# Optimization experiments

Hardware: AMD Instinct MI355X
Metric: run time of the kernel (lower is better)

The kernel has to match this reference:

```python
import jax, jax.numpy as jnp
import numpy as np

E = 8      # num_experts
D = 512    # input feature dim
H1 = 512   # expert_hidden[0]
H2 = 256   # expert_hidden[1]
Y = 256    # y_dim
B = 8192   # batch
ALPHA = 0.2


def setup_inputs() -> dict:
    key = jax.random.key(0)
    ks = jax.random.split(key, 8)
    h = jax.random.normal(ks[0], (B, D), dtype=jnp.float32)
    gate_id = jax.random.randint(ks[1], (B,), 0, E, dtype=jnp.int64)
    # Per-expert MLP parameters, stacked over expert axis (Glorot-ish scale)
    W1 = jax.random.normal(ks[2], (E, D, H1), dtype=jnp.float32) * (1.0 / np.sqrt(D))
    b1 = jnp.zeros((E, H1), dtype=jnp.float32)
    W2 = jax.random.normal(ks[3], (E, H1, H2), dtype=jnp.float32) * (1.0 / np.sqrt(H1))
    b2 = jnp.zeros((E, H2), dtype=jnp.float32)
    W3 = jax.random.normal(ks[4], (E, H2, Y), dtype=jnp.float32) * (1.0 / np.sqrt(H2))
    b3 = jnp.zeros((E, Y), dtype=jnp.float32)
    return {"h": h, "gate_id": gate_id, "W1": W1, "b1": b1,
            "W2": W2, "b2": b2, "W3": W3, "b3": b3}


def _leaky(x):
    return jnp.where(x > 0, x, ALPHA * x)


def reference(h, gate_id, W1, b1, W2, b2, W3, b3):
    # Hard routing: gate_id = clip(round(gate_id), 0, E-1)
    g = jnp.clip(jnp.round(gate_id.astype(jnp.float32)).astype(jnp.int32), 0, E - 1)
    # Dense all-experts compute (jit-friendly, no dynamic shapes), then select
    # the routed expert's output per row. Same math as dispatch/stitch.
    a1 = _leaky(jnp.einsum('bd,edh->ebh', h, W1) + b1[:, None, :])   # [E,B,H1]
    a2 = _leaky(jnp.einsum('ebh,ehk->ebk', a1, W2) + b2[:, None, :]) # [E,B,H2]
    y = jnp.einsum('ebk,eky->eby', a2, W3) + b3[:, None, :]          # [E,B,Y]
    out = y[g, jnp.arange(h.shape[0])]                                # [B,Y]
    return out
```

## Files before the change

kernel.cpp:

```cpp
#include <hip/hip_runtime.h>
#include <stdint.h>

#define NE 8
#define ND 512
#define NH1 512
#define NH2 256
#define NY 256
#define NB 8192
#define BM3 32
#define MAXT3 (NB/BM3 + NE - 1)
#define W1T (NE * (ND/32) * (NH1/32))
#define W2T (NE * (NH1/32) * (NH2/32))
#define W3T (NE * (NH2/32) * (NY/32))
#define WTT (W1T + W2T + W3T)

typedef float f32x4 __attribute__((ext_vector_type(4)));
typedef __bf16 bf16x8 __attribute__((ext_vector_type(8)));
typedef unsigned short u16x8 __attribute__((ext_vector_type(8)));

__device__ __forceinline__ unsigned short f2bf(float f) {
  unsigned int u = __float_as_uint(f);
  u += 0x7fffu + ((u >> 16) & 1u);
  return (unsigned short)(u >> 16);
}

__device__ __forceinline__ int clampe(int g) {
  return g < 0 ? 0 : (g > NE - 1 ? NE - 1 : g);
}



__global__ __launch_bounds__(1024)
void prep_k(const int* __restrict__ gate,
            const float* __restrict__ W1, const float* __restrict__ W2,
            const float* __restrict__ W3,
            unsigned short* __restrict__ w1f, unsigned short* __restrict__ w2f,
            unsigned short* __restrict__ w3f,
            int* __restrict__ meta, int* __restrict__ perm)
{
  __shared__ char sm[36928] __attribute__((aligned(16)));
  int b = blockIdx.x, t = threadIdx.x;

  if (b < WTT) {
    float* tt = (float*)sm;
    const float* src; unsigned short* dst; int K, N, idx;
    if (b < W1T)            { src = W1; dst = w1f; K = ND;  N = NH1; idx = b; }
    else if (b < W1T + W2T) { src = W2; dst = w2f; K = NH1; N = NH2; idx = b - W1T; }
    else                    { src = W3; dst = w3f; K = NH2; N = NY;  idx = b - W1T - W2T; }
    int ntn = N >> 5, ntk = K >> 5;
    int n0 = (idx % ntn) * 32;
    int k0 = ((idx / ntn) % ntk) * 32;
    int g  = idx / (ntn * ntk);
    int tx = t & 31, ty = t >> 5;
    const float* s = src + (size_t)g * K * N;
    tt[ty * 33 + tx] = s[(size_t)(k0 + ty) * N + n0 + tx];
    __syncthreads();
    unsigned short* d = dst + (size_t)g * K * N;
    int j    = t & 7;
    int lane = (t >> 3) & 63;
    int fi   = t >> 9;
    int c    = ((lane >> 4) << 3) | j;
    int i    = (fi << 4) | (lane & 15);
    int kt   = k0 >> 5;
    int f    = (n0 >> 4) + fi;
    d[(((size_t)kt * (N >> 4) + f) * 64 + lane) * 8 + j] = f2bf(tt[c * 33 + i]);
    return;
  }

  unsigned int* lcnt = (unsigned int*)sm;
  int* pre   = (int*)(sm + 4096);
  int* cnt8  = (int*)(sm + 36864);
  int* offs8 = cnt8 + 8;

  int g8[8];
  unsigned int c = 0;
  #pragma unroll
  for (int i = 0; i < 8; i++) {
    int g = clampe(gate[t * 8 + i]);
    g8[i] = g;
    c += 1u << (4 * g);
  }
  lcnt[t] = c;
  __syncthreads();

  int wave = t >> 6, lane = t & 63;
  if (wave < NE) {
    int e = wave;
    int carry = 0;
    for (int ch = 0; ch < 16; ch++) {
      int idx = ch * 64 + lane;
      int v = (int)((lcnt[idx] >> (4 * e)) & 15u);
      int s = v;
      #pragma unroll
      for (int d = 1; d < 64; d <<= 1) {
        int up = __shfl_up(s, d, 64);
        if (lane >= d) s += up;
      }
      pre[e * 1024 + idx] = carry + s - v;
      carry += __shfl(s, 63, 64);
    }
    if (lane == 0) cnt8[e] = carry;
  }
  __syncthreads();

  if (t == 0) {
    int off = 0, tt2 = 0;
    for (int e = 0; e < NE; e++) {
      int cc = cnt8[e];
      meta[e] = cc;
      meta[8 + e] = off;
      offs8[e] = off;
      int ntl = (cc + BM3 - 1) / BM3;
      for (int i = 0; i < ntl; i++) meta[1024 + tt2++] = (e << 16) | i;
      off += cc;
    }
    meta[24] = tt2;
  }
  __syncthreads();

  unsigned int run = 0;
  #pragma unroll
  for (int i = 0; i < 8; i++) {
    int g = g8[i];
    int r = (int)((run >> (4 * g)) & 15u);
    run += 1u << (4 * g);
    perm[offs8[g] + pre[g * 1024 + t] + r] = t * 8 + i;
  }
}

__global__ __launch_bounds__(512, 4)
void mlp_k(const float* __restrict__ h,
           const float* __restrict__ b1, const float* __restrict__ b2,
           const float* __restrict__ b3,
           float* __restrict__ out,
           const int* __restrict__ meta, const int* __restrict__ perm,
           const unsigned short* __restrict__ w1f,
           const unsigned short* __restrict__ w2f,
           const unsigned short* __restrict__ w3f)
{
  __shared__ unsigned short sA[BM3 * 520];
  __shared__ unsigned short sB[BM3 * 520];
  __shared__ int permc[BM3];

  if ((int)blockIdx.x >= meta[24]) return;

  int tid  = threadIdx.x;
  int ent  = meta[1024 + blockIdx.x];
  int e    = ent >> 16;
  int trow = ent & 0xffff;
  int cnt  = meta[e];
  int off  = meta[8 + e];
  int row0 = trow * BM3;

  if (tid < BM3) {
    int grow = row0 + tid;
    permc[tid] = (grow < cnt) ? perm[off + grow] : 0;
  }
  __syncthreads();

  int wave = tid >> 6, lane = tid & 63;
  int lm = lane & 15, quad = lane >> 4;

  {
    int r  = tid >> 4;
    int cb = (tid & 15) * 8;
    const float* hrow = h + (size_t)permc[r] * ND;
    #pragma unroll
    for (int jj = 0; jj < 4; jj++) {
      int col = cb + jj * 128;
      float4 f0 = *(const float4*)(hrow + col);
      float4 f1 = *(const float4*)(hrow + col + 4);
      union { u16x8 v; unsigned short u[8]; } pk;
      pk.u[0] = f2bf(f0.x); pk.u[1] = f2bf(f0.y); pk.u[2] = f2bf(f0.z); pk.u[3] = f2bf(f0.w);
      pk.u[4] = f2bf(f1.x); pk.u[5] = f2bf(f1.y); pk.u[6] = f2bf(f1.z); pk.u[7] = f2bf(f1.w);
      *(u16x8*)(sA + r * 520 + col) = pk.v;
    }
  }
  __syncthreads();

  f32x4 zero = {0.f, 0.f, 0.f, 0.f};

  {
    f32x4 acc[2][4];
    #pragma unroll
    for (int mi = 0; mi < 2; mi++)
      #pragma unroll
      for (int ni = 0; ni < 4; ni++)
        acc[mi][ni] = zero;
    const unsigned short* Wb = w1f + (size_t)e * ND * NH1 + ((size_t)(wave * 4) * 64 + lane) * 8;
    bf16x8 cur[4], nxt[4];
    #pragma unroll
    for (int ni = 0; ni < 4; ni++)
      cur[ni] = *reinterpret_cast<const bf16x8*>(Wb + ni * 512);
    for (int t = 0; t < 16; t++) {
      int tn = (t + 1 < 16) ? t + 1 : t;
      #pragma unroll
      for (int ni = 0; ni < 4; ni++)
        nxt[ni] = *reinterpret_cast<const bf16x8*>(Wb + (size_t)tn * 16384 + ni * 512);
      bf16x8 af[2];
      #pragma unroll
      for (int mi = 0; mi < 2; mi++)
        af[mi] = *reinterpret_cast<const bf16x8*>(sA + (mi * 16 + lm) * 520 + t * 32 + quad * 8);
      #pragma unroll
      for (int mi = 0; mi < 2; mi++)
        #pragma unroll
        for (int ni = 0; ni < 4; ni++)
          acc[mi][ni] = __builtin_amdgcn_mfma_f32_16x16x32_bf16(af[mi], cur[ni], acc[mi][ni], 0, 0, 0);
      #pragma unroll
      for (int ni = 0; ni < 4; ni++)
        cur[ni] = nxt[ni];
    }
    #pragma unroll
    for (int mi = 0; mi < 2; mi++)
      #pragma unroll
      for (int ni = 0; ni < 4; ni++) {
        int col = (wave * 4 + ni) * 16 + lm;
        float bv = b1[e * NH1 + col];
        #pragma unroll
        for (int r = 0; r < 4; r++) {
          int row = mi * 16 + quad * 4 + r;
          float v = acc[mi][ni][r] + bv;
          v = (v > 0.f) ? v : 0.2f * v;
          sB[row * 520 + col] = f2bf(v);
        }
      }
  }
  __syncthreads();

  {
    f32x4 acc[2][2];
    #pragma unroll
    for (int mi = 0; mi < 2; mi++)
      #pragma unroll
      for (int ni = 0; ni < 2; ni++)
        acc[mi][ni] = zero;
    const unsigned short* Wb = w2f + (size_t)e * NH1 * NH2 + ((size_t)(wave * 2) * 64 + lane) * 8;
    bf16x8 cur[2], nxt[2];
    #pragma unroll
    for (int ni = 0; ni < 2; ni++)
      cur[ni] = *reinterpret_cast<const bf16x8*>(Wb + ni * 512);
    for (int t = 0; t < 16; t++) {
      int tn = (t + 1 < 16) ? t + 1 : t;
      #pragma unroll
      for (int ni = 0; ni < 2; ni++)
        nxt[ni] = *reinterpret_cast<const bf16x8*>(Wb + (size_t)tn * 8192 + ni * 512);
      bf16x8 af[2];
      #pragma unroll
      for (int mi = 0; mi < 2; mi++)
        af[mi] = *reinterpret_cast<const bf16x8*>(sB + (mi * 16 + lm) * 520 + t * 32 + quad * 8);
      #pragma unroll
      for (int mi = 0; mi < 2; mi++)
        #pragma unroll
        for (int ni = 0; ni < 2; ni++)
          acc[mi][ni] = __builtin_amdgcn_mfma_f32_16x16x32_bf16(af[mi], cur[ni], acc[mi][ni], 0, 0, 0);
      #pragma unroll
      for (int ni = 0; ni < 2; ni++)
        cur[ni] = nxt[ni];
    }
    #pragma unroll
    for (int mi = 0; mi < 2; mi++)
      #pragma unroll
      for (int ni = 0; ni < 2; ni++) {
        int col = (wave * 2 + ni) * 16 + lm;
        float bv = b2[e * NH2 + col];
        #pragma unroll
        for (int r = 0; r < 4; r++) {
          int row = mi * 16 + quad * 4 + r;
          float v = acc[mi][ni][r] + bv;
          v = (v > 0.f) ? v : 0.2f * v;
          sA[row * 264 + col] = f2bf(v);
        }
      }
  }
  __syncthreads();

  {
    f32x4 acc[2][2];
    #pragma unroll
    for (int mi = 0; mi < 2; mi++)
      #pragma unroll
      for (int ni = 0; ni < 2; ni++)
        acc[mi][ni] = zero;
    const unsigned short* Wb = w3f + (size_t)e * NH2 * NY + ((size_t)(wave * 2) * 64 + lane) * 8;
    bf16x8 cur[2], nxt[2];
    #pragma unroll
    for (int ni = 0; ni < 2; ni++)
      cur[ni] = *reinterpret_cast<const bf16x8*>(Wb + ni * 512);
    for (int t = 0; t < 8; t++) {
      int tn = (t + 1 < 8) ? t + 1 : t;
      #pragma unroll
      for (int ni = 0; ni < 2; ni++)
        nxt[ni] = *reinterpret_cast<const bf16x8*>(Wb + (size_t)tn * 8192 + ni * 512);
      bf16x8 af[2];
      #pragma unroll
      for (int mi = 0; mi < 2; mi++)
        af[mi] = *reinterpret_cast<const bf16x8*>(sA + (mi * 16 + lm) * 264 + t * 32 + quad * 8);
      #pragma unroll
      for (int mi = 0; mi < 2; mi++)
        #pragma unroll
        for (int ni = 0; ni < 2; ni++)
          acc[mi][ni] = __builtin_amdgcn_mfma_f32_16x16x32_bf16(af[mi], cur[ni], acc[mi][ni], 0, 0, 0);
      #pragma unroll
      for (int ni = 0; ni < 2; ni++)
        cur[ni] = nxt[ni];
    }
    #pragma unroll
    for (int mi = 0; mi < 2; mi++)
      #pragma unroll
      for (int ni = 0; ni < 2; ni++) {
        int col = (wave * 2 + ni) * 16 + lm;
        float bv = b3[e * NY + col];
        #pragma unroll
        for (int r = 0; r < 4; r++) {
          int row = mi * 16 + quad * 4 + r;
          int grow = row0 + row;
          if (grow < cnt) {
            float v = acc[mi][ni][r] + bv;
            out[(size_t)permc[row] * NY + col] = v;
          }
        }
      }
  }
}

extern "C" void kernel_launch(void* const* d_in, const int* in_sizes, int n_in,
                              void* d_out, int out_size, void* d_ws, size_t ws_size,
                              hipStream_t stream) {
  (void)in_sizes; (void)n_in; (void)out_size; (void)ws_size;
  const float* h  = (const float*)d_in[0];
  const int* gate = (const int*)d_in[1];
  const float* W1 = (const float*)d_in[2];
  const float* b1 = (const float*)d_in[3];
  const float* W2 = (const float*)d_in[4];
  const float* b2 = (const float*)d_in[5];
  const float* W3 = (const float*)d_in[6];
  const float* b3 = (const float*)d_in[7];
  float* out = (float*)d_out;

  char* ws = (char*)d_ws;
  int* meta = (int*)ws;
  int* perm = (int*)(ws + 8192);
  unsigned short* w1f = (unsigned short*)(ws + 8192 + 32768);
  unsigned short* w2f = w1f + (size_t)NE * ND * NH1;
  unsigned short* w3f = w2f + (size_t)NE * NH1 * NH2;

  prep_k<<<WTT + 1, 1024, 0, stream>>>(gate, W1, W2, W3, w1f, w2f, w3f, meta, perm);
  mlp_k<<<MAXT3, 512, 0, stream>>>(h, b1, b2, b3, out, meta, perm, w1f, w2f, w3f);
}
```

Before: 124.8 us.

## Deepen weight prefetch to two stages and prefetch next-layer weights early

The weight-fragment pipeline goes from one stage to two stages, with all k-loops fully unrolled. The first weight fragments of the next layer are loaded before the bias/activation epilogue and barrier, so their latency hides behind the epilogue. The shared permc array and its barrier are removed: each thread reads its perm index directly and issues the h row loads alongside the first W1 loads. The costs are more registers, which may hurt occupancy under launch_bounds(512,4), and repeated perm reads in the output store.

```diff
diff --git a/kernel.cpp b/kernel.cpp
--- a/kernel.cpp
+++ b/kernel.cpp
@@ -140,7 +140,6 @@
 {
   __shared__ unsigned short sA[BM3 * 520];
   __shared__ unsigned short sB[BM3 * 520];
-  __shared__ int permc[BM3];
 
   if ((int)blockIdx.x >= meta[24]) return;
 
@@ -152,175 +151,180 @@
   int off  = meta[8 + e];
   int row0 = trow * BM3;
 
-  if (tid < BM3) {
-    int grow = row0 + tid;
-    permc[tid] = (grow < cnt) ? perm[off + grow] : 0;
-  }
-  __syncthreads();
-
   int wave = tid >> 6, lane = tid & 63;
   int lm = lane & 15, quad = lane >> 4;
 
-  {
-    int r  = tid >> 4;
-    int cb = (tid & 15) * 8;
-    const float* hrow = h + (size_t)permc[r] * ND;
-    #pragma unroll
-    for (int jj = 0; jj < 4; jj++) {
-      int col = cb + jj * 128;
-      float4 f0 = *(const float4*)(hrow + col);
-      float4 f1 = *(const float4*)(hrow + col + 4);
-      union { u16x8 v; unsigned short u[8]; } pk;
-      pk.u[0] = f2bf(f0.x); pk.u[1] = f2bf(f0.y); pk.u[2] = f2bf(f0.z); pk.u[3] = f2bf(f0.w);
-      pk.u[4] = f2bf(f1.x); pk.u[5] = f2bf(f1.y); pk.u[6] = f2bf(f1.z); pk.u[7] = f2bf(f1.w);
-      *(u16x8*)(sA + r * 520 + col) = pk.v;
-    }
+  const unsigned short* W1b = w1f + (size_t)e * ND * NH1 + ((size_t)(wave * 4) * 64 + lane) * 8;
+  const unsigned short* W2b = w2f + (size_t)e * NH1 * NH2 + ((size_t)(wave * 2) * 64 + lane) * 8;
+  const unsigned short* W3b = w3f + (size_t)e * NH2 * NY + ((size_t)(wave * 2) * 64 + lane) * 8;
+
+  int r  = tid >> 4;
+  int cb = (tid & 15) * 8;
+  int grow_g = row0 + r;
+  int prow = 0;
+  if (grow_g < cnt) prow = perm[off + grow_g];
+  const float* hrow = h + (size_t)prow * ND;
+  float4 hv[8];
+  #pragma unroll
+  for (int jj = 0; jj < 4; jj++) {
+    hv[2 * jj]     = *(const float4*)(hrow + cb + jj * 128);
+    hv[2 * jj + 1] = *(const float4*)(hrow + cb + jj * 128 + 4);
+  }
+
+  bf16x8 c0[4], c1[4], c2[4];
+  #pragma unroll
+  for (int ni = 0; ni < 4; ni++)
+    c0[ni] = *reinterpret_cast<const bf16x8*>(W1b + ni * 512);
+  #pragma unroll
+  for (int ni = 0; ni < 4; ni++)
+    c1[ni] = *reinterpret_cast<const bf16x8*>(W1b + 16384 + ni * 512);
+
+  #pragma unroll
+  for (int jj = 0; jj < 4; jj++) {
+    union { u16x8 v; unsigned short u[8]; } pk;
+    float4 f0 = hv[2 * jj], f1 = hv[2 * jj + 1];
+    pk.u[0] = f2bf(f0.x); pk.u[1] = f2bf(f0.y); pk.u[2] = f2bf(f0.z); pk.u[3] = f2bf(f0.w);
+    pk.u[4] = f2bf(f1.x); pk.u[5] = f2bf(f1.y); pk.u[6] = f2bf(f1.z); pk.u[7] = f2bf(f1.w);
+    *(u16x8*)(sA + r * 520 + cb + jj * 128) = pk.v;
   }
   __syncthreads();
 
   f32x4 zero = {0.f, 0.f, 0.f, 0.f};
 
-  {
-    f32x4 acc[2][4];
+  f32x4 acc1[2][4];
+  #pragma unroll
+  for (int mi = 0; mi < 2; mi++)
+    #pragma unroll
+    for (int ni = 0; ni < 4; ni++)
+      acc1[mi][ni] = zero;
+  #pragma unroll
+  for (int t = 0; t < 16; t++) {
+    int tp = (t + 2 < 16) ? t + 2 : 15;
+    #pragma unroll
+    for (int ni = 0; ni < 4; ni++)
+      c2[ni] = *reinterpret_cast<const bf16x8*>(W1b + (size_t)tp * 16384 + ni * 512);
+    bf16x8 af[2];
+    #pragma unroll
+    for (int mi = 0; mi < 2; mi++)
+      af[mi] = *reinterpret_cast<const bf16x8*>(sA + (mi * 16 + lm) * 520 + t * 32 + quad * 8);
     #pragma unroll
     for (int mi = 0; mi < 2; mi++)
       #pragma unroll
       for (int ni = 0; ni < 4; ni++)
-        acc[mi][ni] = zero;
-    const unsigned short* Wb = w1f + (size_t)e * ND * NH1 + ((size_t)(wave * 4) * 64 + lane) * 8;
-    bf16x8 cur[4], nxt[4];
-    #pragma unroll
-    for (int ni = 0; ni < 4; ni++)
-      cur[ni] = *reinterpret_cast<const bf16x8*>(Wb + ni * 512);
-    for (int t = 0; t < 16; t++) {
-      int tn = (t + 1 < 16) ? t + 1 : t;
-      #pragma unroll
-      for (int ni = 0; ni < 4; ni++)
-        nxt[ni] = *reinterpret_cast<const bf16x8*>(Wb + (size_t)tn * 16384 + ni * 512);
-      bf16x8 af[2];
-      #pragma unroll
-      for (int mi = 0; mi < 2; mi++)
-        af[mi] = *reinterpret_cast<const bf16x8*>(sA + (mi * 16 + lm) * 520 + t * 32 + quad * 8);
-      #pragma unroll
-      for (int mi = 0; mi < 2; mi++)
-        #pragma unroll
-        for (int ni = 0; ni < 4; ni++)
-          acc[mi][ni] = __builtin_amdgcn_mfma_f32_16x16x32_bf16(af[mi], cur[ni], acc[mi][ni], 0, 0, 0);
-      #pragma unroll
-      for (int ni = 0; ni < 4; ni++)
-        cur[ni] = nxt[ni];
-    }
-    #pragma unroll
-    for (int mi = 0; mi < 2; mi++)
-      #pragma unroll
-      for (int ni = 0; ni < 4; ni++) {
-        int col = (wave * 4 + ni) * 16 + lm;
-        float bv = b1[e * NH1 + col];
-        #pragma unroll
-        for (int r = 0; r < 4; r++) {
-          int row = mi * 16 + quad * 4 + r;
-          float v = acc[mi][ni][r] + bv;
-          v = (v > 0.f) ? v : 0.2f * v;
-          sB[row * 520 + col] = f2bf(v);
+        acc1[mi][ni] = __builtin_amdgcn_mfma_f32_16x16x32_bf16(af[mi], c0[ni], acc1[mi][ni], 0, 0, 0);
+    #pragma unroll
+    for (int ni = 0; ni < 4; ni++) { c0[ni] = c1[ni]; c1[ni] = c2[ni]; }
+  }
+  bf16x8 d0[2], d1[2], d2[2];
+  #pragma unroll
+  for (int ni = 0; ni < 2; ni++)
+    d0[ni] = *reinterpret_cast<const bf16x8*>(W2b + ni * 512);
+  #pragma unroll
+  for (int ni = 0; ni < 2; ni++)
+    d1[ni] = *reinterpret_cast<const bf16x8*>(W2b + 8192 + ni * 512);
+  #pragma unroll
+  for (int mi = 0; mi < 2; mi++)
+    #pragma unroll
+    for (int ni = 0; ni < 4; ni++) {
+      int col = (wave * 4 + ni) * 16 + lm;
+      float bv = b1[e * NH1 + col];
+      #pragma unroll
+      for (int rr = 0; rr < 4; rr++) {
+        int row = mi * 16 + quad * 4 + rr;
+        float v = acc1[mi][ni][rr] + bv;
+        v = (v > 0.f) ? v : 0.2f * v;
+        sB[row * 520 + col] = f2bf(v);
+      }
+    }
+  __syncthreads();
+
+  f32x4 acc2[2][2];
+  #pragma unroll
+  for (int mi = 0; mi < 2; mi++)
+    #pragma unroll
+    for (int ni = 0; ni < 2; ni++)
+      acc2[mi][ni] = zero;
+  #pragma unroll
+  for (int t = 0; t < 16; t++) {
+    int tp = (t + 2 < 16) ? t + 2 : 15;
+    #pragma unroll
+    for (int ni = 0; ni < 2; ni++)
+      d2[ni] = *reinterpret_cast<const bf16x8*>(W2b + (size_t)tp * 8192 + ni * 512);
+    bf16x8 af[2];
+    #pragma unroll
+    for (int mi = 0; mi < 2; mi++)
+      af[mi] = *reinterpret_cast<const bf16x8*>(sB + (mi * 16 + lm) * 520 + t * 32 + quad * 8);
+    #pragma unroll
+    for (int mi = 0; mi < 2; mi++)
+      #pragma unroll
+      for (int ni = 0; ni < 2; ni++)
+        acc2[mi][ni] = __builtin_amdgcn_mfma_f32_16x16x32_bf16(af[mi], d0[ni], acc2[mi][ni], 0, 0, 0);
+    #pragma unroll
+    for (int ni = 0; ni < 2; ni++) { d0[ni] = d1[ni]; d1[ni] = d2[ni]; }
+  }
+  bf16x8 g0[2], g1[2], g2[2];
+  #pragma unroll
+  for (int ni = 0; ni < 2; ni++)
+    g0[ni] = *reinterpret_cast<const bf16x8*>(W3b + ni * 512);
+  #pragma unroll
+  for (int ni = 0; ni < 2; ni++)
+    g1[ni] = *reinterpret_cast<const bf16x8*>(W3b + 8192 + ni * 512);
+  #pragma unroll
+  for (int mi = 0; mi < 2; mi++)
+    #pragma unroll
+    for (int ni = 0; ni < 2; ni++) {
+      int col = (wave * 2 + ni) * 16 + lm;
+      float bv = b2[e * NH2 + col];
+      #pragma unroll
+      for (int rr = 0; rr < 4; rr++) {
+        int row = mi * 16 + quad * 4 + rr;
+        float v = acc2[mi][ni][rr] + bv;
+        v = (v > 0.f) ? v : 0.2f * v;
+        sA[row * 264 + col] = f2bf(v);
+      }
+    }
+  __syncthreads();
+
+  f32x4 acc3[2][2];
+  #pragma unroll
+  for (int mi = 0; mi < 2; mi++)
+    #pragma unroll
+    for (int ni = 0; ni < 2; ni++)
+      acc3[mi][ni] = zero;
+  #pragma unroll
+  for (int t = 0; t < 8; t++) {
+    int tp = (t + 2 < 8) ? t + 2 : 7;
+    #pragma unroll
+    for (int ni = 0; ni < 2; ni++)
+      g2[ni] = *reinterpret_cast<const bf16x8*>(W3b + (size_t)tp * 8192 + ni * 512);
+    bf16x8 af[2];
+    #pragma unroll
+    for (int mi = 0; mi < 2; mi++)
+      af[mi] = *reinterpret_cast<const bf16x8*>(sA + (mi * 16 + lm) * 264 + t * 32 + quad * 8);
+    #pragma unroll
+    for (int mi = 0; mi < 2; mi++)
+      #pragma unroll
+      for (int ni = 0; ni < 2; ni++)
+        acc3[mi][ni] = __builtin_amdgcn_mfma_f32_16x16x32_bf16(af[mi], g0[ni], acc3[mi][ni], 0, 0, 0);
+    #pragma unroll
+    for (int ni = 0; ni < 2; ni++) { g0[ni] = g1[ni]; g1[ni] = g2[ni]; }
+  }
+  #pragma unroll
+  for (int mi = 0; mi < 2; mi++)
+    #pragma unroll
+    for (int ni = 0; ni < 2; ni++) {
+      int col = (wave * 2 + ni) * 16 + lm;
+      float bv = b3[e * NY + col];
+      #pragma unroll
+      for (int rr = 0; rr < 4; rr++) {
+        int row = mi * 16 + quad * 4 + rr;
+        int grow = row0 + row;
+        if (grow < cnt) {
+          float v = acc3[mi][ni][rr] + bv;
+          out[(size_t)perm[off + grow] * NY + col] = v;
         }
       }
-  }
-  __syncthreads();
-
-  {
-    f32x4 acc[2][2];
-    #pragma unroll
-    for (int mi = 0; mi < 2; mi++)
-      #pragma unroll
-      for (int ni = 0; ni < 2; ni++)
-        acc[mi][ni] = zero;
-    const unsigned short* Wb = w2f + (size_t)e * NH1 * NH2 + ((size_t)(wave * 2) * 64 + lane) * 8;
-    bf16x8 cur[2], nxt[2];
-    #pragma unroll
-    for (int ni = 0; ni < 2; ni++)
-      cur[ni] = *reinterpret_cast<const bf16x8*>(Wb + ni * 512);
-    for (int t = 0; t < 16; t++) {
-      int tn = (t + 1 < 16) ? t + 1 : t;
-      #pragma unroll
-      for (int ni = 0; ni < 2; ni++)
-        nxt[ni] = *reinterpret_cast<const bf16x8*>(Wb + (size_t)tn * 8192 + ni * 512);
-      bf16x8 af[2];
-      #pragma unroll
-      for (int mi = 0; mi < 2; mi++)
-        af[mi] = *reinterpret_cast<const bf16x8*>(sB + (mi * 16 + lm) * 520 + t * 32 + quad * 8);
-      #pragma unroll
-      for (int mi = 0; mi < 2; mi++)
-        #pragma unroll
-        for (int ni = 0; ni < 2; ni++)
-          acc[mi][ni] = __builtin_amdgcn_mfma_f32_16x16x32_bf16(af[mi], cur[ni], acc[mi][ni], 0, 0, 0);
-      #pragma unroll
-      for (int ni = 0; ni < 2; ni++)
-        cur[ni] = nxt[ni];
-    }
-    #pragma unroll
-    for (int mi = 0; mi < 2; mi++)
-      #pragma unroll
-      for (int ni = 0; ni < 2; ni++) {
-        int col = (wave * 2 + ni) * 16 + lm;
-        float bv = b2[e * NH2 + col];
-        #pragma unroll
-        for (int r = 0; r < 4; r++) {
-          int row = mi * 16 + quad * 4 + r;
-          float v = acc[mi][ni][r] + bv;
-          v = (v > 0.f) ? v : 0.2f * v;
-          sA[row * 264 + col] = f2bf(v);
-        }
-      }
-  }
-  __syncthreads();
-
-  {
-    f32x4 acc[2][2];
-    #pragma unroll
-    for (int mi = 0; mi < 2; mi++)
-      #pragma unroll
-      for (int ni = 0; ni < 2; ni++)
-        acc[mi][ni] = zero;
-    const unsigned short* Wb = w3f + (size_t)e * NH2 * NY + ((size_t)(wave * 2) * 64 + lane) * 8;
-    bf16x8 cur[2], nxt[2];
-    #pragma unroll
-    for (int ni = 0; ni < 2; ni++)
-      cur[ni] = *reinterpret_cast<const bf16x8*>(Wb + ni * 512);
-    for (int t = 0; t < 8; t++) {
-      int tn = (t + 1 < 8) ? t + 1 : t;
-      #pragma unroll
-      for (int ni = 0; ni < 2; ni++)
-        nxt[ni] = *reinterpret_cast<const bf16x8*>(Wb + (size_t)tn * 8192 + ni * 512);
-      bf16x8 af[2];
-      #pragma unroll
-      for (int mi = 0; mi < 2; mi++)
-        af[mi] = *reinterpret_cast<const bf16x8*>(sA + (mi * 16 + lm) * 264 + t * 32 + quad * 8);
-      #pragma unroll
-      for (int mi = 0; mi < 2; mi++)
-        #pragma unroll
-        for (int ni = 0; ni < 2; ni++)
-          acc[mi][ni] = __builtin_amdgcn_mfma_f32_16x16x32_bf16(af[mi], cur[ni], acc[mi][ni], 0, 0, 0);
-      #pragma unroll
-      for (int ni = 0; ni < 2; ni++)
-        cur[ni] = nxt[ni];
-    }
-    #pragma unroll
-    for (int mi = 0; mi < 2; mi++)
-      #pragma unroll
-      for (int ni = 0; ni < 2; ni++) {
-        int col = (wave * 2 + ni) * 16 + lm;
-        float bv = b3[e * NY + col];
-        #pragma unroll
-        for (int r = 0; r < 4; r++) {
-          int row = mi * 16 + quad * 4 + r;
-          int grow = row0 + row;
-          if (grow < cnt) {
-            float v = acc[mi][ni][r] + bv;
-            out[(size_t)permc[row] * NY + col] = v;
-          }
-        }
-      }
-  }
+    }
 }
 
 extern "C" void kernel_launch(void* const* d_in, const int* in_sizes, int n_in,
```

Result: slower. 131.2 us (+5.1%).
